# Performance work log

Hardware: AMD Instinct MI355X
Metric: run time of the kernel (lower is better)

Reference implementation:

```python
import jax, jax.numpy as jnp
import numpy as np

LEAKY_SLOPE = 0.01  # torch nn.LeakyReLU default

def _mlp(x, w1, b1, w2, b2):
    # MLP_Layer(num_layers=2, batch_norm=False): Linear -> ReLU -> Linear
    return jax.nn.relu(x @ w1 + b1) @ w2 + b2

def _edge_softmax(scores, dst, num_nodes):
    # softmax over incoming edges of each destination node; scores: [E, H]
    m = jax.ops.segment_max(scores, dst, num_segments=num_nodes)  # [N, H]
    e = jnp.exp(scores - m[dst])
    s = jax.ops.segment_sum(e, dst, num_segments=num_nodes)       # [N, H]
    return e / s[dst]

def setup_inputs() -> dict:
    key = jax.random.key(0)
    ks = jax.random.split(key, 10)
    N, E, H = 50000, 800000, 4
    D_H, PCA, PI, HID = 64, 64, 32, 128
    inp = {
        "h":    jax.random.normal(ks[0], (N, D_H), jnp.float32),
        "pca":  jax.random.normal(ks[1], (N, PCA), jnp.float32),
        "pimg": jax.random.normal(ks[2], (N, PI), jnp.float32),
        "pca_w1": jax.random.normal(ks[3], (2 * PCA, HID), jnp.float32) * (1.0 / np.sqrt(2 * PCA)),
        "pca_b1": jnp.zeros((HID,), jnp.float32),
        "pca_w2": jax.random.normal(ks[4], (HID, H), jnp.float32) * (1.0 / np.sqrt(HID)),
        "pca_b2": jnp.zeros((H,), jnp.float32),
        "pi_w1": jax.random.normal(ks[5], (2 * PI, HID), jnp.float32) * (1.0 / np.sqrt(2 * PI)),
        "pi_b1": jnp.zeros((HID,), jnp.float32),
        "pi_w2": jax.random.normal(ks[6], (HID, H), jnp.float32) * (1.0 / np.sqrt(HID)),
        "pi_b2": jnp.zeros((H,), jnp.float32),
        "src": jax.random.randint(ks[7], (E,), 0, N, jnp.int32),
        "dst": jax.random.randint(ks[8], (E,), 0, N, jnp.int32),
    }
    return inp

def reference(h, pca, pimg, pca_w1, pca_b1, pca_w2, pca_b2,
              pi_w1, pi_b1, pi_w2, pi_b2, src, dst):
    N = h.shape[0]

    def attend(feat, w1, b1, w2, b2):
        e_feat = jnp.concatenate([feat[src], feat[dst]], axis=1)        # [E, 2F]
        score = jax.nn.leaky_relu(_mlp(e_feat, w1, b1, w2, b2), LEAKY_SLOPE)  # [E, H]
        a = _edge_softmax(score, dst, N)                                # [E, H]
        msg = h[src][:, None, :] * a[:, :, None]                        # [E, H, D]
        return jax.ops.segment_sum(msg, dst, num_segments=N)           # [N, H, D]

    out_pca = attend(pca, pca_w1, pca_b1, pca_w2, pca_b2)
    out_pi = attend(pimg, pi_w1, pi_b1, pi_w2, pi_b2)
    return jnp.concatenate([out_pca, out_pi], axis=-1)                  # [N, H, 2D]
```

## Files before the change

### kernel.cpp

```cpp
#include <hip/hip_runtime.h>
#include <hip/hip_fp16.h>

constexpr int HID = 128;
constexpr int DH  = 64;

typedef _Float16 f16x2 __attribute__((ext_vector_type(2)));
typedef _Float16 fh8   __attribute__((ext_vector_type(8)));
typedef float    f32x4v __attribute__((ext_vector_type(4)));

__device__ __forceinline__ fh8 relu8(fh8 x) {
  fh8 z = {0, 0, 0, 0, 0, 0, 0, 0};
#if __has_builtin(__builtin_elementwise_max)
  return __builtin_elementwise_max(x, z);
#else
  fh8 r;
#pragma unroll
  for (int i = 0; i < 8; i++) r[i] = x[i] > z[i] ? x[i] : z[i];
  return r;
#endif
}

__global__ void frag_setup_kernel(const float* __restrict__ w1a, const float* __restrict__ w1b,
                                  _Float16* __restrict__ fragTab) {
  int flat = blockIdx.x * 256 + threadIdx.x;
  if (flat >= 32768) return;
  int rel = flat >> 14;
  int r2 = flat & 16383;
  int g = r2 >> 10, s = (r2 >> 9) & 1, l = (r2 >> 3) & 63, j = r2 & 7;
  int bc = l & 15, bkg = l >> 4;
  int k = s * 32 + bkg * 8 + j;
  int F = rel ? 32 : 64;
  const float* w1 = rel ? w1b : w1a;
  float val = 0.f;
  if (k < F) {
    int jout = (g & 7) * 16 + bc;
    int krow = (g < 8) ? k : (F + k);
    val = w1[krow * HID + jout];
  }
  fragTab[flat] = (_Float16)val;
}

__launch_bounds__(256)
__global__ void uv_mfma_kernel(const float* __restrict__ pca, const float* __restrict__ pimg,
                               const float* __restrict__ b1a, const float* __restrict__ b1b,
                               const _Float16* __restrict__ fragTab,
                               _Float16* __restrict__ u_cat, _Float16* __restrict__ v_cat, int N) {
  __shared__ _Float16 sB[16384];
  int rel = blockIdx.y;
  const float* feat = rel ? pimg : pca;
  const float* b1   = rel ? b1b : b1a;
  int F  = rel ? 32 : 64;
  int KS = rel ? 1 : 2;
  int tid = threadIdx.x;
  {
    const fh8* srcp = (const fh8*)(fragTab + rel * 16384);
    fh8* dstp = (fh8*)sB;
    for (int i = tid; i < 2048; i += 256) dstp[i] = srcp[i];
  }
  __syncthreads();
  int lane = tid & 63, w = tid >> 6;
  int r = lane & 15, kg = lane >> 4;
  int node = blockIdx.x * 64 + w * 16 + r;
  int nclamp = node < N ? node : N - 1;
  fh8 a[2];
#pragma unroll
  for (int s = 0; s < 2; s++) {
    if (s < KS) {
      const float* fp = feat + (size_t)nclamp * F + s * 32 + kg * 8;
      float4 f0 = *(const float4*)fp;
      float4 f1 = *(const float4*)(fp + 4);
      fh8 t;
      t[0] = (_Float16)f0.x; t[1] = (_Float16)f0.y; t[2] = (_Float16)f0.z; t[3] = (_Float16)f0.w;
      t[4] = (_Float16)f1.x; t[5] = (_Float16)f1.y; t[6] = (_Float16)f1.z; t[7] = (_Float16)f1.w;
      a[s] = t;
    }
  }
  int onode0 = blockIdx.x * 64 + w * 16 + kg * 4;
  int c = lane & 15;
#pragma unroll
  for (int g = 0; g < 16; g++) {
    f32x4v acc = {0.f, 0.f, 0.f, 0.f};
    acc = __builtin_amdgcn_mfma_f32_16x16x32_f16(a[0], ((const fh8*)sB)[(g * 2 + 0) * 64 + lane], acc, 0, 0, 0);
    if (KS == 2)
      acc = __builtin_amdgcn_mfma_f32_16x16x32_f16(a[1], ((const fh8*)sB)[(g * 2 + 1) * 64 + lane], acc, 0, 0, 0);
    bool isv = g >= 8;
    int jout = (g & 7) * 16 + c;
    float bias = isv ? b1[jout] : 0.f;
    _Float16* outp = isv ? v_cat : u_cat;
    size_t colix = (size_t)rel * 128 + jout;
#pragma unroll
    for (int q = 0; q < 4; q++) {
      int on = onode0 + q;
      if (on < N) outp[(size_t)on * 256 + colix] = (_Float16)(acc[q] + bias);
    }
  }
}

__global__ void count_h16_kernel(const int* __restrict__ dst, int* __restrict__ counts, int E,
                                 const float* __restrict__ h, _Float16* __restrict__ h16, int total) {
  int i = blockIdx.x * 256 + threadIdx.x;
  if (i < E) atomicAdd(&counts[dst[i]], 1);
  int base = i * 8;
  if (base + 7 < total) {
    float4 f0 = *(const float4*)(h + base);
    float4 f1 = *(const float4*)(h + base + 4);
    fh8 t;
    t[0] = (_Float16)f0.x; t[1] = (_Float16)f0.y; t[2] = (_Float16)f0.z; t[3] = (_Float16)f0.w;
    t[4] = (_Float16)f1.x; t[5] = (_Float16)f1.y; t[6] = (_Float16)f1.z; t[7] = (_Float16)f1.w;
    *(fh8*)(h16 + base) = t;
  }
}

__launch_bounds__(256)
__global__ void scan1_kernel(const int* __restrict__ counts, int* __restrict__ bsums, int N) {
  int b = blockIdx.x, tid = threadIdx.x;
  int base = b * 1024 + tid * 4;
  int s = 0;
  if (base + 3 < N) {
    int4 v = *(const int4*)(counts + base);
    s = v.x + v.y + v.z + v.w;
  } else {
    for (int q = 0; q < 4; q++) { int idx = base + q; if (idx < N) s += counts[idx]; }
  }
#pragma unroll
  for (int o = 32; o >= 1; o >>= 1) s += __shfl_xor(s, o);
  __shared__ int ws[4];
  if ((tid & 63) == 0) ws[tid >> 6] = s;
  __syncthreads();
  if (tid == 0) bsums[b] = ws[0] + ws[1] + ws[2] + ws[3];
}

__launch_bounds__(1024)
__global__ void scan2_kernel(const int* __restrict__ bsums, int* __restrict__ bpre,
                             int* __restrict__ offsets, int NB, int N, int E) {
  int tid = threadIdx.x, lane = tid & 63, w = tid >> 6;
  int v = (tid < NB) ? bsums[tid] : 0;
  int incl = v;
#pragma unroll
  for (int o = 1; o < 64; o <<= 1) { int t = __shfl_up(incl, o); if (lane >= o) incl += t; }
  __shared__ int ws[16];
  if (lane == 63) ws[w] = incl;
  __syncthreads();
  int wpre = 0;
  for (int q = 0; q < w; q++) wpre += ws[q];
  if (tid < NB) bpre[tid] = wpre + incl - v;
  if (tid == 0) offsets[N] = E;
}

__launch_bounds__(256)
__global__ void scan3_kernel(const int* __restrict__ counts, const int* __restrict__ bpre,
                             int* __restrict__ offsets, int N) {
  int b = blockIdx.x, tid = threadIdx.x, lane = tid & 63, w = tid >> 6;
  int base = b * 1024 + tid * 4;
  int c[4] = {0, 0, 0, 0};
  if (base + 3 < N) {
    int4 v = *(const int4*)(counts + base);
    c[0] = v.x; c[1] = v.y; c[2] = v.z; c[3] = v.w;
  } else {
    for (int q = 0; q < 4; q++) { int idx = base + q; if (idx < N) c[q] = counts[idx]; }
  }
  int s = c[0] + c[1] + c[2] + c[3];
  int incl = s;
#pragma unroll
  for (int o = 1; o < 64; o <<= 1) { int t = __shfl_up(incl, o); if (lane >= o) incl += t; }
  int excl = incl - s;
  __shared__ int ws[4];
  if (lane == 63) ws[w] = incl;
  __syncthreads();
  int wpre = 0;
  for (int q = 0; q < w; q++) wpre += ws[q];
  int off = bpre[b] + wpre + excl;
  for (int q = 0; q < 4; q++) {
    int idx = base + q;
    if (idx < N) offsets[idx] = off;
    off += c[q];
  }
}

__global__ void fill_kernel(const int* __restrict__ src, const int* __restrict__ dst,
                            int* __restrict__ cursor, int2* __restrict__ edges, int E) {
  int e = blockIdx.x * 256 + threadIdx.x;
  if (e < E) {
    int d = dst[e];
    int pos = atomicAdd(&cursor[d], 1);
    edges[pos] = make_int2(src[e], d);
  }
}

__launch_bounds__(256, 8)
__global__ void score_kernel(const _Float16* __restrict__ u_cat, const _Float16* __restrict__ v_cat,
                             const int2* __restrict__ edges,
                             const float* __restrict__ w2a, const float* __restrict__ w2b,
                             const float* __restrict__ b2a, const float* __restrict__ b2b,
                             _Float16* __restrict__ ek, int E) {
  __shared__ _Float16 sB[8 * 64 * 8];
  int tid = threadIdx.x, lane = tid & 63, w = tid >> 6;
  int col = lane & 15, kg = lane >> 4;
  for (int idx = tid; idx < 4096; idx += 256) {
    int t = idx >> 9, l = (idx >> 3) & 63, j = idx & 7;
    int bc = l & 15;
    int k = t * 32 + ((l >> 4) << 3) + j;
    float val = 0.f;
    if (bc < 4) { if (k < 128) val = w2a[k * 4 + bc]; }
    else if (bc < 8) { if (k >= 128) val = w2b[(k - 128) * 4 + (bc - 4)]; }
    sB[idx] = (_Float16)val;
  }
  __syncthreads();

  int ebase = blockIdx.x * 256 + w * 64;
  const _Float16* up[4];
  const _Float16* vp[4];
#pragma unroll
  for (int m = 0; m < 4; m++) {
    int em = ebase + m * 16 + col;
    int ec = em < E ? em : 0;
    int2 sd = edges[ec];
    up[m] = u_cat + (size_t)sd.x * 256 + kg * 8;
    vp[m] = v_cat + (size_t)sd.y * 256 + kg * 8;
  }

  f32x4v acc[4];
#pragma unroll
  for (int m = 0; m < 4; m++) acc[m] = (f32x4v){0.f, 0.f, 0.f, 0.f};

#pragma unroll
  for (int t = 0; t < 8; t++) {
    fh8 bf = *(const fh8*)(sB + ((t * 64 + lane) << 3));
#pragma unroll
    for (int m = 0; m < 4; m++) {
      fh8 uu = *(const fh8*)(up[m] + t * 32);
      fh8 vv = *(const fh8*)(vp[m] + t * 32);
      acc[m] = __builtin_amdgcn_mfma_f32_16x16x32_f16(relu8(uu + vv), bf, acc[m], 0, 0, 0);
    }
  }

  if (col < 8) {
    float b2v = (col < 4) ? b2a[col] : b2b[col - 4];
#pragma unroll
    for (int m = 0; m < 4; m++) {
#pragma unroll
      for (int q = 0; q < 4; q++) {
        int er = ebase + m * 16 + kg * 4 + q;
        if (er < E) {
          float x = acc[m][q] + b2v;
          x = x > 0.f ? x : 0.01f * x;
          ek[(size_t)er * 8 + col] = (_Float16)__expf(x);
        }
      }
    }
  }
}

__launch_bounds__(256, 8)
__global__ void agg_kernel(const _Float16* __restrict__ ek, const int2* __restrict__ edges,
                           const int* __restrict__ offsets, const _Float16* __restrict__ h16,
                           float* __restrict__ out, int N) {
  int wid = blockIdx.x * 4 + (threadIdx.x >> 6);
  int lane = threadIdx.x & 63;
  if (wid >= N) return;
  int off0 = offsets[wid], off1 = offsets[wid + 1];
  int deg = off1 - off0;
  float* op = out + (size_t)wid * 512;
  if (deg == 0) {
#pragma unroll
    for (int k = 0; k < 4; k++) { op[k * 128 + lane] = 0.f; op[k * 128 + 64 + lane] = 0.f; }
    return;
  }
  float accO[8] = {0, 0, 0, 0, 0, 0, 0, 0};
  float ssum[8] = {0, 0, 0, 0, 0, 0, 0, 0};
  int last = off1 - 1;
  for (int jj = 0; jj < deg; jj += 4) {
    int i0 = off0 + jj;
    int i1 = min(i0 + 1, last), i2 = min(i0 + 2, last), i3 = min(i0 + 3, last);
    bool m1 = jj + 1 < deg, m2 = jj + 2 < deg, m3 = jj + 3 < deg;
    int s0 = edges[i0].x, s1 = edges[i1].x, s2 = edges[i2].x, s3 = edges[i3].x;
    fh8 e0 = *(const fh8*)(ek + (size_t)i0 * 8);
    fh8 e1 = *(const fh8*)(ek + (size_t)i1 * 8);
    fh8 e2 = *(const fh8*)(ek + (size_t)i2 * 8);
    fh8 e3 = *(const fh8*)(ek + (size_t)i3 * 8);
    float hv0 = (float)h16[(size_t)s0 * DH + lane];
    float hv1 = (float)h16[(size_t)s1 * DH + lane];
    float hv2 = (float)h16[(size_t)s2 * DH + lane];
    float hv3 = (float)h16[(size_t)s3 * DH + lane];
#pragma unroll
    for (int k = 0; k < 8; k++) {
      float e0v = (float)e0[k];
      float e1v = m1 ? (float)e1[k] : 0.f;
      float e2v = m2 ? (float)e2[k] : 0.f;
      float e3v = m3 ? (float)e3[k] : 0.f;
      accO[k] = fmaf(e0v, hv0, accO[k]);
      accO[k] = fmaf(e1v, hv1, accO[k]);
      accO[k] = fmaf(e2v, hv2, accO[k]);
      accO[k] = fmaf(e3v, hv3, accO[k]);
      ssum[k] += (e0v + e1v) + (e2v + e3v);
    }
  }
#pragma unroll
  for (int k = 0; k < 8; k++) {
    float rsv = 1.f / ssum[k];
    int colo = k < 4 ? k * 128 + lane : (k - 4) * 128 + 64 + lane;
    op[colo] = accO[k] * rsv;
  }
}

extern "C" void kernel_launch(void* const* d_in, const int* in_sizes, int n_in,
                              void* d_out, int out_size, void* d_ws, size_t ws_size,
                              hipStream_t stream) {
  const float* h      = (const float*)d_in[0];
  const float* pca    = (const float*)d_in[1];
  const float* pimg   = (const float*)d_in[2];
  const float* pca_w1 = (const float*)d_in[3];
  const float* pca_b1 = (const float*)d_in[4];
  const float* pca_w2 = (const float*)d_in[5];
  const float* pca_b2 = (const float*)d_in[6];
  const float* pi_w1  = (const float*)d_in[7];
  const float* pi_b1  = (const float*)d_in[8];
  const float* pi_w2  = (const float*)d_in[9];
  const float* pi_b2  = (const float*)d_in[10];
  const int*   src    = (const int*)d_in[11];
  const int*   dst    = (const int*)d_in[12];
  int N = in_sizes[0] / 64;
  int E = in_sizes[11];
  float* out = (float*)d_out;

  char* ws = (char*)d_ws;
  size_t o = 0;
  auto alloc = [&](size_t bytes) { void* p = ws + o; o += (bytes + 255) & ~(size_t)255; return p; };
  _Float16* u_cat  = (_Float16*)alloc((size_t)N * 256 * 2);
  _Float16* v_cat  = (_Float16*)alloc((size_t)N * 256 * 2);
  _Float16* h16    = (_Float16*)alloc((size_t)N * 64 * 2);
  _Float16* fragTab = (_Float16*)alloc(32768 * 2);
  int* counts  = (int*)alloc((size_t)N * 4);
  int* cursor  = (int*)alloc((size_t)N * 4);
  int* offsets = (int*)alloc((size_t)(N + 1) * 4);
  int* bsums   = (int*)alloc(1024 * 4);
  int* bpre    = (int*)alloc(1024 * 4);
  int2* edges  = (int2*)alloc((size_t)E * 8);
  _Float16* ekb = (_Float16*)alloc((size_t)E * 8 * 2);

  hipMemsetAsync(counts, 0, (size_t)N * 4, stream);

  frag_setup_kernel<<<128, 256, 0, stream>>>(pca_w1, pi_w1, fragTab);
  count_h16_kernel<<<(E + 255) / 256, 256, 0, stream>>>(dst, counts, E, h, h16, N * 64);
  dim3 uvgrid((N + 63) / 64, 2);
  uv_mfma_kernel<<<uvgrid, 256, 0, stream>>>(pca, pimg, pca_b1, pi_b1, fragTab, u_cat, v_cat, N);
  int NB = (N + 1023) / 1024;
  scan1_kernel<<<NB, 256, 0, stream>>>(counts, bsums, N);
  scan2_kernel<<<1, 1024, 0, stream>>>(bsums, bpre, offsets, NB, N, E);
  scan3_kernel<<<NB, 256, 0, stream>>>(counts, bpre, offsets, N);
  hipMemcpyAsync(cursor, offsets, (size_t)N * 4, hipMemcpyDeviceToDevice, stream);
  fill_kernel<<<(E + 255) / 256, 256, 0, stream>>>(src, dst, cursor, edges, E);
  score_kernel<<<(E + 255) / 256, 256, 0, stream>>>(u_cat, v_cat, edges,
                                                    pca_w2, pi_w2, pca_b2, pi_b2, ekb, E);
  agg_kernel<<<(N + 3) / 4, 256, 0, stream>>>(ekb, edges, offsets, h16, out, N);
}
```

Measured before the change: 290.1 us.

## Fuse setup and scan kernels, transpose MFMA output, prefetch edge sources

Folds the weight-fragment setup into the uv MFMA kernel, which builds the fp16 weight tile in shared memory directly. It also swaps the MFMA operands so each lane writes four contiguous fp16 outputs in one vector store. The scan2 and scan3 kernels and the cursor memcpy are merged into one kernel that does the block-prefix scan in a wavefront and writes both offsets and cursor. The aggregation loop now prefetches the next four edge source indices one iteration ahead. Together these cut launch count and scattered stores, at the cost of every uv block rebuilding the weight tile and a 64-block limit on the fused scan.

```diff
diff --git a/kernel.cpp b/kernel.cpp
--- a/kernel.cpp
+++ b/kernel.cpp
@@ -5,6 +5,7 @@
 constexpr int DH  = 64;
 
 typedef _Float16 f16x2 __attribute__((ext_vector_type(2)));
+typedef _Float16 fh4   __attribute__((ext_vector_type(4)));
 typedef _Float16 fh8   __attribute__((ext_vector_type(8)));
 typedef float    f32x4v __attribute__((ext_vector_type(4)));
 
@@ -18,82 +19,6 @@
   for (int i = 0; i < 8; i++) r[i] = x[i] > z[i] ? x[i] : z[i];
   return r;
 #endif
-}
-
-__global__ void frag_setup_kernel(const float* __restrict__ w1a, const float* __restrict__ w1b,
-                                  _Float16* __restrict__ fragTab) {
-  int flat = blockIdx.x * 256 + threadIdx.x;
-  if (flat >= 32768) return;
-  int rel = flat >> 14;
-  int r2 = flat & 16383;
-  int g = r2 >> 10, s = (r2 >> 9) & 1, l = (r2 >> 3) & 63, j = r2 & 7;
-  int bc = l & 15, bkg = l >> 4;
-  int k = s * 32 + bkg * 8 + j;
-  int F = rel ? 32 : 64;
-  const float* w1 = rel ? w1b : w1a;
-  float val = 0.f;
-  if (k < F) {
-    int jout = (g & 7) * 16 + bc;
-    int krow = (g < 8) ? k : (F + k);
-    val = w1[krow * HID + jout];
-  }
-  fragTab[flat] = (_Float16)val;
-}
-
-__launch_bounds__(256)
-__global__ void uv_mfma_kernel(const float* __restrict__ pca, const float* __restrict__ pimg,
-                               const float* __restrict__ b1a, const float* __restrict__ b1b,
-                               const _Float16* __restrict__ fragTab,
-                               _Float16* __restrict__ u_cat, _Float16* __restrict__ v_cat, int N) {
-  __shared__ _Float16 sB[16384];
-  int rel = blockIdx.y;
-  const float* feat = rel ? pimg : pca;
-  const float* b1   = rel ? b1b : b1a;
-  int F  = rel ? 32 : 64;
-  int KS = rel ? 1 : 2;
-  int tid = threadIdx.x;
-  {
-    const fh8* srcp = (const fh8*)(fragTab + rel * 16384);
-    fh8* dstp = (fh8*)sB;
-    for (int i = tid; i < 2048; i += 256) dstp[i] = srcp[i];
-  }
-  __syncthreads();
-  int lane = tid & 63, w = tid >> 6;
-  int r = lane & 15, kg = lane >> 4;
-  int node = blockIdx.x * 64 + w * 16 + r;
-  int nclamp = node < N ? node : N - 1;
-  fh8 a[2];
-#pragma unroll
-  for (int s = 0; s < 2; s++) {
-    if (s < KS) {
-      const float* fp = feat + (size_t)nclamp * F + s * 32 + kg * 8;
-      float4 f0 = *(const float4*)fp;
-      float4 f1 = *(const float4*)(fp + 4);
-      fh8 t;
-      t[0] = (_Float16)f0.x; t[1] = (_Float16)f0.y; t[2] = (_Float16)f0.z; t[3] = (_Float16)f0.w;
-      t[4] = (_Float16)f1.x; t[5] = (_Float16)f1.y; t[6] = (_Float16)f1.z; t[7] = (_Float16)f1.w;
-      a[s] = t;
-    }
-  }
-  int onode0 = blockIdx.x * 64 + w * 16 + kg * 4;
-  int c = lane & 15;
-#pragma unroll
-  for (int g = 0; g < 16; g++) {
-    f32x4v acc = {0.f, 0.f, 0.f, 0.f};
-    acc = __builtin_amdgcn_mfma_f32_16x16x32_f16(a[0], ((const fh8*)sB)[(g * 2 + 0) * 64 + lane], acc, 0, 0, 0);
-    if (KS == 2)
-      acc = __builtin_amdgcn_mfma_f32_16x16x32_f16(a[1], ((const fh8*)sB)[(g * 2 + 1) * 64 + lane], acc, 0, 0, 0);
-    bool isv = g >= 8;
-    int jout = (g & 7) * 16 + c;
-    float bias = isv ? b1[jout] : 0.f;
-    _Float16* outp = isv ? v_cat : u_cat;
-    size_t colix = (size_t)rel * 128 + jout;
-#pragma unroll
-    for (int q = 0; q < 4; q++) {
-      int on = onode0 + q;
-      if (on < N) outp[(size_t)on * 256 + colix] = (_Float16)(acc[q] + bias);
-    }
-  }
 }
 
 __global__ void count_h16_kernel(const int* __restrict__ dst, int* __restrict__ counts, int E,
@@ -112,6 +37,73 @@
 }
 
 __launch_bounds__(256)
+__global__ void uv_mfma_kernel(const float* __restrict__ pca, const float* __restrict__ pimg,
+                               const float* __restrict__ b1a, const float* __restrict__ b1b,
+                               const float* __restrict__ w1a, const float* __restrict__ w1b,
+                               _Float16* __restrict__ u_cat, _Float16* __restrict__ v_cat, int N) {
+  __shared__ _Float16 sB[16384];
+  int rel = blockIdx.y;
+  const float* feat = rel ? pimg : pca;
+  const float* b1   = rel ? b1b : b1a;
+  const float* w1   = rel ? w1b : w1a;
+  int F  = rel ? 32 : 64;
+  int KS = rel ? 1 : 2;
+  int tid = threadIdx.x;
+  for (int idx = tid; idx < 16384; idx += 256) {
+    int g = idx >> 10, s = (idx >> 9) & 1, l = (idx >> 3) & 63, j = idx & 7;
+    int bc = l & 15, bkg = l >> 4;
+    int k = s * 32 + bkg * 8 + j;
+    float val = 0.f;
+    if (k < F) {
+      int jslot = (g & 7) * 16 + bc;
+      int krow = (g < 8) ? k : (F + k);
+      val = w1[krow * HID + jslot];
+    }
+    sB[idx] = (_Float16)val;
+  }
+  __syncthreads();
+  int lane = tid & 63, w = tid >> 6;
+  int c = lane & 15, kg = lane >> 4;
+  int node = blockIdx.x * 64 + w * 16 + c;
+  int nclamp = node < N ? node : N - 1;
+  fh8 bfeat[2];
+#pragma unroll
+  for (int s = 0; s < 2; s++) {
+    if (s < KS) {
+      const float* fp = feat + (size_t)nclamp * F + s * 32 + kg * 8;
+      float4 f0 = *(const float4*)fp;
+      float4 f1 = *(const float4*)(fp + 4);
+      fh8 t;
+      t[0] = (_Float16)f0.x; t[1] = (_Float16)f0.y; t[2] = (_Float16)f0.z; t[3] = (_Float16)f0.w;
+      t[4] = (_Float16)f1.x; t[5] = (_Float16)f1.y; t[6] = (_Float16)f1.z; t[7] = (_Float16)f1.w;
+      bfeat[s] = t;
+    }
+  }
+  float4 b1q[8];
+#pragma unroll
+  for (int g = 0; g < 8; g++) b1q[g] = *(const float4*)(b1 + g * 16 + kg * 4);
+
+  bool wr = node < N;
+#pragma unroll
+  for (int g = 0; g < 16; g++) {
+    f32x4v acc = {0.f, 0.f, 0.f, 0.f};
+    acc = __builtin_amdgcn_mfma_f32_16x16x32_f16(((const fh8*)sB)[(g * 2 + 0) * 64 + lane], bfeat[0], acc, 0, 0, 0);
+    if (KS == 2)
+      acc = __builtin_amdgcn_mfma_f32_16x16x32_f16(((const fh8*)sB)[(g * 2 + 1) * 64 + lane], bfeat[1], acc, 0, 0, 0);
+    bool isv = g >= 8;
+    int jbase = (g & 7) * 16 + kg * 4;
+    float4 bias = isv ? b1q[g & 7] : make_float4(0.f, 0.f, 0.f, 0.f);
+    fh4 pk;
+    pk[0] = (_Float16)(acc[0] + bias.x);
+    pk[1] = (_Float16)(acc[1] + bias.y);
+    pk[2] = (_Float16)(acc[2] + bias.z);
+    pk[3] = (_Float16)(acc[3] + bias.w);
+    _Float16* outp = isv ? v_cat : u_cat;
+    if (wr) *(fh4*)(outp + (size_t)node * 256 + rel * 128 + jbase) = pk;
+  }
+}
+
+__launch_bounds__(256)
 __global__ void scan1_kernel(const int* __restrict__ counts, int* __restrict__ bsums, int N) {
   int b = blockIdx.x, tid = threadIdx.x;
   int base = b * 1024 + tid * 4;
@@ -130,27 +122,22 @@
   if (tid == 0) bsums[b] = ws[0] + ws[1] + ws[2] + ws[3];
 }
 
-__launch_bounds__(1024)
-__global__ void scan2_kernel(const int* __restrict__ bsums, int* __restrict__ bpre,
-                             int* __restrict__ offsets, int NB, int N, int E) {
-  int tid = threadIdx.x, lane = tid & 63, w = tid >> 6;
-  int v = (tid < NB) ? bsums[tid] : 0;
-  int incl = v;
-#pragma unroll
-  for (int o = 1; o < 64; o <<= 1) { int t = __shfl_up(incl, o); if (lane >= o) incl += t; }
-  __shared__ int ws[16];
-  if (lane == 63) ws[w] = incl;
-  __syncthreads();
-  int wpre = 0;
-  for (int q = 0; q < w; q++) wpre += ws[q];
-  if (tid < NB) bpre[tid] = wpre + incl - v;
-  if (tid == 0) offsets[N] = E;
-}
-
 __launch_bounds__(256)
-__global__ void scan3_kernel(const int* __restrict__ counts, const int* __restrict__ bpre,
-                             int* __restrict__ offsets, int N) {
+__global__ void scan23_kernel(const int* __restrict__ counts, const int* __restrict__ bsums,
+                              int* __restrict__ offsets, int* __restrict__ cursor,
+                              int NB, int N, int E) {
   int b = blockIdx.x, tid = threadIdx.x, lane = tid & 63, w = tid >> 6;
+  __shared__ int s_bpre;
+  if (tid < 64) {
+    int v = (lane < NB) ? bsums[lane] : 0;
+    int incl = v;
+#pragma unroll
+    for (int o = 1; o < 64; o <<= 1) { int t = __shfl_up(incl, o); if (lane >= o) incl += t; }
+    int excl = incl - v;
+    int t = __shfl(excl, b);
+    if (lane == 0) s_bpre = t;
+  }
+  __syncthreads();
   int base = b * 1024 + tid * 4;
   int c[4] = {0, 0, 0, 0};
   if (base + 3 < N) {
@@ -169,12 +156,13 @@
   __syncthreads();
   int wpre = 0;
   for (int q = 0; q < w; q++) wpre += ws[q];
-  int off = bpre[b] + wpre + excl;
+  int off = s_bpre + wpre + excl;
   for (int q = 0; q < 4; q++) {
     int idx = base + q;
-    if (idx < N) offsets[idx] = off;
+    if (idx < N) { offsets[idx] = off; cursor[idx] = off; }
     off += c[q];
   }
+  if (b == 0 && tid == 0) offsets[N] = E;
 }
 
 __global__ void fill_kernel(const int* __restrict__ src, const int* __restrict__ dst,
@@ -269,11 +257,14 @@
   float accO[8] = {0, 0, 0, 0, 0, 0, 0, 0};
   float ssum[8] = {0, 0, 0, 0, 0, 0, 0, 0};
   int last = off1 - 1;
+  int s0 = edges[off0].x;
+  int s1 = edges[min(off0 + 1, last)].x;
+  int s2 = edges[min(off0 + 2, last)].x;
+  int s3 = edges[min(off0 + 3, last)].x;
   for (int jj = 0; jj < deg; jj += 4) {
     int i0 = off0 + jj;
     int i1 = min(i0 + 1, last), i2 = min(i0 + 2, last), i3 = min(i0 + 3, last);
     bool m1 = jj + 1 < deg, m2 = jj + 2 < deg, m3 = jj + 3 < deg;
-    int s0 = edges[i0].x, s1 = edges[i1].x, s2 = edges[i2].x, s3 = edges[i3].x;
     fh8 e0 = *(const fh8*)(ek + (size_t)i0 * 8);
     fh8 e1 = *(const fh8*)(ek + (size_t)i1 * 8);
     fh8 e2 = *(const fh8*)(ek + (size_t)i2 * 8);
@@ -282,6 +273,10 @@
     float hv1 = (float)h16[(size_t)s1 * DH + lane];
     float hv2 = (float)h16[(size_t)s2 * DH + lane];
     float hv3 = (float)h16[(size_t)s3 * DH + lane];
+    int t0 = edges[min(i0 + 4, last)].x;
+    int t1 = edges[min(i0 + 5, last)].x;
+    int t2 = edges[min(i0 + 6, last)].x;
+    int t3 = edges[min(i0 + 7, last)].x;
 #pragma unroll
     for (int k = 0; k < 8; k++) {
       float e0v = (float)e0[k];
@@ -294,6 +289,7 @@
       accO[k] = fmaf(e3v, hv3, accO[k]);
       ssum[k] += (e0v + e1v) + (e2v + e3v);
     }
+    s0 = t0; s1 = t1; s2 = t2; s3 = t3;
   }
 #pragma unroll
   for (int k = 0; k < 8; k++) {
@@ -329,26 +325,21 @@
   _Float16* u_cat  = (_Float16*)alloc((size_t)N * 256 * 2);
   _Float16* v_cat  = (_Float16*)alloc((size_t)N * 256 * 2);
   _Float16* h16    = (_Float16*)alloc((size_t)N * 64 * 2);
-  _Float16* fragTab = (_Float16*)alloc(32768 * 2);
   int* counts  = (int*)alloc((size_t)N * 4);
   int* cursor  = (int*)alloc((size_t)N * 4);
   int* offsets = (int*)alloc((size_t)(N + 1) * 4);
   int* bsums   = (int*)alloc(1024 * 4);
-  int* bpre    = (int*)alloc(1024 * 4);
   int2* edges  = (int2*)alloc((size_t)E * 8);
   _Float16* ekb = (_Float16*)alloc((size_t)E * 8 * 2);
 
   hipMemsetAsync(counts, 0, (size_t)N * 4, stream);
 
-  frag_setup_kernel<<<128, 256, 0, stream>>>(pca_w1, pi_w1, fragTab);
   count_h16_kernel<<<(E + 255) / 256, 256, 0, stream>>>(dst, counts, E, h, h16, N * 64);
   dim3 uvgrid((N + 63) / 64, 2);
-  uv_mfma_kernel<<<uvgrid, 256, 0, stream>>>(pca, pimg, pca_b1, pi_b1, fragTab, u_cat, v_cat, N);
+  uv_mfma_kernel<<<uvgrid, 256, 0, stream>>>(pca, pimg, pca_b1, pi_b1, pca_w1, pi_w1, u_cat, v_cat, N);
   int NB = (N + 1023) / 1024;
   scan1_kernel<<<NB, 256, 0, stream>>>(counts, bsums, N);
-  scan2_kernel<<<1, 1024, 0, stream>>>(bsums, bpre, offsets, NB, N, E);
-  scan3_kernel<<<NB, 256, 0, stream>>>(counts, bpre, offsets, N);
-  hipMemcpyAsync(cursor, offsets, (size_t)N * 4, hipMemcpyDeviceToDevice, stream);
+  scan23_kernel<<<NB, 256, 0, stream>>>(counts, bsums, offsets, cursor, NB, N, E);
   fill_kernel<<<(E + 255) / 256, 256, 0, stream>>>(src, dst, cursor, edges, E);
   score_kernel<<<(E + 255) / 256, 256, 0, stream>>>(u_cat, v_cat, edges,
                                                     pca_w2, pi_w2, pca_b2, pi_b2, ekb, E);
```

Result: slower. 304.8 us (+5.0%).
